# Performance work log

Hardware: AMD Instinct MI355X
Metric: run time of the kernel (lower is better)

## Reference

```python
import jax, jax.numpy as jnp
import numpy as np

D = 64        # kg_embedding_dim
T = 4096      # tokens
N = 20000     # kg nodes
M = T + N     # total nodes
E = 100000    # edges
R = 50        # relation types (num_edge_embeddings)
V = 100000    # num_node_embeddings
TOK = 768     # token_embedding_size


def setup_inputs() -> dict:
    key = jax.random.key(0)
    ks = jax.random.split(key, 24)
    s = 0.05
    node_ids = jax.random.randint(ks[0], (N,), 0, V)
    edge_index = jax.random.randint(ks[1], (2, E), 0, M)
    rel_ids = jax.random.randint(ks[2], (E,), 0, R)
    edge_attr = jax.nn.one_hot(rel_ids, R, dtype=jnp.float32)  # [E,R]
    token_embeddings = jax.random.normal(ks[3], (T, TOK), dtype=jnp.float32)
    node_type_labels = jax.random.randint(ks[4], (M,), 0, 3)
    return {
        'node_ids': node_ids,
        'edge_index': edge_index,
        'edge_attr': edge_attr,
        'token_embeddings': token_embeddings,
        'node_type_labels': node_type_labels,
        # learned params
        'kg_emb': jax.random.normal(ks[5], (V, D), dtype=jnp.float32) * s,
        'rel_emb': jax.random.normal(ks[6], (R, D), dtype=jnp.float32) * s,
        'w_e2': jax.random.normal(ks[7], (D, D * D), dtype=jnp.float32) * s,
        'b_e2': jnp.zeros((D * D,), dtype=jnp.float32),
        'att1_w': jax.random.normal(ks[8], (2 * D, 1), dtype=jnp.float32) * s,
        'att1_b': jnp.zeros((1,), dtype=jnp.float32),
        'root1': jax.random.normal(ks[9], (D, D), dtype=jnp.float32) * s,
        'bias1': jnp.zeros((D,), dtype=jnp.float32),
        'att2_w': jax.random.normal(ks[10], (2 * D, 1), dtype=jnp.float32) * s,
        'att2_b': jnp.zeros((1,), dtype=jnp.float32),
        'root2': jax.random.normal(ks[11], (D, D), dtype=jnp.float32) * s,
        'bias2': jnp.zeros((D,), dtype=jnp.float32),
        'w_lin1': jax.random.normal(ks[12], (TOK, D), dtype=jnp.float32) * s,
        'b_lin1': jnp.zeros((D,), dtype=jnp.float32),
        'w_lin2': jax.random.normal(ks[13], (D, TOK), dtype=jnp.float32) * s,
        'b_lin2': jnp.zeros((TOK,), dtype=jnp.float32),
        'w_nt': jax.random.normal(ks[14], (D, 3), dtype=jnp.float32) * s,
        'b_nt': jnp.zeros((3,), dtype=jnp.float32),
    }


def _ecgat(x, src, dst, w_edge, att_w, att_b, root, bias):
    # x: [M,D], w_edge: [E,D,D]
    x_j = x[src]                                    # gather source nodes [E,D]
    x_i = x[dst]                                    # gather target nodes [E,D]
    nbr = jnp.einsum('ed,edo->eo', x_j, w_edge)     # per-edge matmul [E,D]
    a = jnp.concatenate([x_i, nbr], axis=1) @ att_w + att_b   # [E,1]
    a = jax.nn.softmax(a, axis=0)                   # global softmax over edges (dim=0 in torch)
    msg = x_j * a                                   # message = x_j * alpha
    aggr = jax.ops.segment_sum(msg, dst, num_segments=M)      # scatter-add [M,D]
    return aggr + x @ root + bias


def reference(node_ids, edge_index, edge_attr, token_embeddings, node_type_labels,
              kg_emb, rel_emb, w_e2, b_e2,
              att1_w, att1_b, root1, bias1,
              att2_w, att2_b, root2, bias2,
              w_lin1, b_lin1, w_lin2, b_lin2, w_nt, b_nt):
    src, dst = edge_index[0], edge_index[1]
    tok = token_embeddings @ w_lin1 + b_lin1        # [T,D]
    nodes = kg_emb[node_ids]                        # [N,D]
    x = jnp.concatenate([tok, nodes], axis=0)       # [M,D]

    # EdgeNet (shared by both conv layers, same edge_attr -> compute once)
    e_emb = edge_attr @ rel_emb                     # [E,D]
    w_edge = jax.nn.relu(e_emb @ w_e2 + b_e2).reshape(E, D, D)  # [E,D,D]

    x1 = _ecgat(x, src, dst, w_edge, att1_w, att1_b, root1, bias1)
    h = jax.nn.relu(x1)                             # dropout = identity in eval
    final_x = _ecgat(h, src, dst, w_edge, att2_w, att2_b, root2, bias2)

    # link_pred loss (MSE, masked, mean over all elements)
    pred_tails = final_x[src] + e_emb
    edge_labels = final_x[dst]
    mask = (edge_attr[:, -3:].sum(axis=1) == 0).astype(final_x.dtype)[:, None]
    kge_loss = jnp.mean((pred_tails - edge_labels) ** 2 * mask)

    # node-type classification loss (cross entropy)
    logp = jax.nn.log_softmax(final_x @ w_nt + b_nt, axis=-1)
    nt_loss = -jnp.mean(jnp.take_along_axis(logp, node_type_labels[:, None], axis=1))

    final_outputs = final_x @ w_lin2 + b_lin2       # [M,TOK]
    return final_outputs, kge_loss, nt_loss
```

## Files before the change

kernel.cpp:

```cpp
#include <hip/hip_runtime.h>

#define Dd   64
#define Tt   4096
#define Nn   20000
#define Mm   24096
#define Ee   100000
#define Rr   50
#define TOK  768

#define NB_TOK   512
#define NB_NODES 1250
#define NB_RELID 4883
#define NB_W     800
#define NB_ZERO  95
#define NBM_HIST 391
#define NBM_U    13
#define NBM_P    6024
#define NBA_FILL 391
#define NBA_ATT  2048
#define NKGE     391
#define NNT      95
#define NFIN     (NKGE+NNT)
#define NGEMM    753

__device__ __forceinline__ float waveRed(float v){
  #pragma unroll
  for(int o=32;o;o>>=1) v += __shfl_xor(v,o,64);
  return v;
}

__global__ __launch_bounds__(256) void k_prep(
    const float* __restrict__ A, const float* __restrict__ wl1, const float* __restrict__ bl1,
    const int* __restrict__ ids, const float* __restrict__ kg,
    const float* __restrict__ ea, int* __restrict__ relid,
    const float* __restrict__ rel, const float* __restrict__ w2, const float* __restrict__ b2,
    float* __restrict__ W, int* __restrict__ deg, float* __restrict__ S,
    float* __restrict__ x){
  __shared__ float As[8*TOK];
  int b = blockIdx.x;
  const int t = threadIdx.x, lane = t&63, wave = t>>6;
  if(b < NB_TOK){
    const int rbase = b*8;
    #pragma unroll
    for(int i=0;i<6;i++){
      int f = t + 256*i;
      int row = f/192, c4 = (f - row*192)*4;
      *(float4*)&As[row*TOK + c4] = *(const float4*)&A[(size_t)(rbase+row)*TOK + c4];
    }
    __syncthreads();
    const int r0 = wave*2, r1 = r0+1;
    float a0=bl1[lane], a1=a0, c0=0.f, c1=0.f;
    for(int k=0;k<TOK;k+=2){
      float w0 = wl1[(size_t)k*Dd + lane];
      float w1 = wl1[(size_t)(k+1)*Dd + lane];
      a0 += As[r0*TOK+k]*w0;  c0 += As[r0*TOK+k+1]*w1;
      a1 += As[r1*TOK+k]*w0;  c1 += As[r1*TOK+k+1]*w1;
    }
    x[(size_t)(rbase+r0)*Dd + lane] = a0+c0;
    x[(size_t)(rbase+r1)*Dd + lane] = a1+c1;
  } else if(b < NB_TOK+NB_NODES){
    int tt = (b-NB_TOK)*256 + t;
    int i = tt>>4, c = tt&15;
    ((float4*)x)[(size_t)(Tt+i)*16 + c] = ((const float4*)kg)[(size_t)ids[i]*16 + c];
  } else if(b < NB_TOK+NB_NODES+NB_RELID){
    int tt = (b-NB_TOK-NB_NODES)*256 + t;
    size_t g4 = (size_t)tt*4;
    if(g4 < (size_t)Ee*Rr){
      float4 v = *(const float4*)&ea[g4];
      #pragma unroll
      for(int j=0;j<4;j++){
        if(((const float*)&v)[j] > 0.5f){
          unsigned g = (unsigned)(g4 + j);
          unsigned e = g / 50u;
          relid[e] = (int)(g - e*50u);
        }
      }
    }
  } else if(b < NB_TOK+NB_NODES+NB_RELID+NB_W){
    int tt = (b-NB_TOK-NB_NODES-NB_RELID)*256 + t;
    int r = tt>>12, j = tt&4095;
    float acc = b2[j];
    const float* rp = rel + r*Dd;
    #pragma unroll 8
    for(int d=0;d<Dd;d++) acc += rp[d] * w2[(size_t)d*4096 + j];
    W[tt] = acc > 0.f ? acc : 0.f;
  } else {
    int tt = (b-NB_TOK-NB_NODES-NB_RELID-NB_W)*256 + t;
    if(tt < Mm) deg[tt] = 0;
    else if(tt < Mm+8) S[tt-Mm] = 0.f;
  }
}

__global__ __launch_bounds__(256) void k_mid(const int* __restrict__ ei,
    int* __restrict__ deg, const float* __restrict__ W,
    const float* __restrict__ a1w, const float* __restrict__ a2w,
    float* __restrict__ U1, float* __restrict__ U2,
    const float* __restrict__ x, float* __restrict__ p){
  int b = blockIdx.x;
  const int t = threadIdx.x, lane = t&63, wave = t>>6;
  if(b < NBM_HIST){
    int e = b*256 + t;
    if(e < Ee) atomicAdd(&deg[ei[Ee+e]], 1);
  } else if(b < NBM_HIST+NBM_U){
    int tt = (b-NBM_HIST)*256 + t;
    if(tt < Rr*Dd){
      const float* wp = W + (size_t)(tt>>6)*4096 + (size_t)(tt&63)*Dd;
      float s1 = 0.f, s2 = 0.f;
      #pragma unroll 8
      for(int o=0;o<Dd;o++){ float w = wp[o]; s1 += w*a1w[Dd+o]; s2 += w*a2w[Dd+o]; }
      U1[tt] = s1; U2[tt] = s2;
    }
  } else {
    int i = (b-NBM_HIST-NBM_U)*4 + wave;
    float pv = waveRed(x[(size_t)i*Dd + lane] * a1w[lane]);
    if(lane==0) p[i] = pv;
  }
}

__global__ __launch_bounds__(1024) void k_scan(const int* __restrict__ deg,
    int* __restrict__ rowptr, int* __restrict__ cursor){
  __shared__ int ts[1024];
  int t = threadIdx.x;
  int base = t*24;
  int loc[24];
  int s = 0;
  #pragma unroll
  for(int j=0;j<24;j++){
    int idx = base+j;
    int d = (idx < Mm) ? deg[idx] : 0;
    loc[j] = s; s += d;
  }
  ts[t] = s;
  __syncthreads();
  for(int off=1; off<1024; off<<=1){
    int add = (t>=off) ? ts[t-off] : 0;
    __syncthreads();
    ts[t] += add;
    __syncthreads();
  }
  int excl = ts[t] - s;
  #pragma unroll
  for(int j=0;j<24;j++){
    int idx = base+j;
    if(idx < Mm){ int v = excl + loc[j]; rowptr[idx] = v; cursor[idx] = v; }
  }
  if(t==1023) rowptr[Mm] = ts[1023];
}

__global__ __launch_bounds__(256) void k_attf(const float* __restrict__ x,
    const int* __restrict__ ei, const int* __restrict__ relid,
    const float* __restrict__ U, const float* __restrict__ p,
    const float* __restrict__ ab, float* __restrict__ expa, float* __restrict__ S,
    int* __restrict__ cursor, int* __restrict__ eidx,
    int dorelu, int dofill){
  __shared__ float sw[4];
  int b = blockIdx.x;
  if(dofill){
    if(b < NBA_FILL){
      int e = b*256 + threadIdx.x;
      if(e < Ee){
        int d = ei[Ee+e];
        int pos = atomicAdd(&cursor[d], 1);
        eidx[pos] = e;
      }
      return;
    }
    b -= NBA_FILL;
  }
  int lane = threadIdx.x&63, wid = threadIdx.x>>6;
  int gw = b*4 + wid;
  float ab0 = ab[0];
  float acc = 0.f;
  for(int e = gw; e < Ee; e += 4*NBA_ATT){
    int src = ei[e], dst = ei[Ee+e], r = relid[e];
    float xv = x[(size_t)src*Dd + lane];
    if(dorelu) xv = fmaxf(xv, 0.f);
    float v = waveRed(xv * U[r*Dd + lane]);
    float ex = expf(v + p[dst] + ab0);
    if(lane==0) expa[e] = ex;
    acc += ex;
  }
  if(lane==0) sw[wid] = acc;
  __syncthreads();
  if(threadIdx.x==0) atomicAdd(S, sw[0]+sw[1]+sw[2]+sw[3]);
}

__global__ __launch_bounds__(256) void k_aggr(const float* __restrict__ x,
    const int* __restrict__ ei, const int* __restrict__ rowptr,
    const int* __restrict__ eidx, const float* __restrict__ expa,
    const float* __restrict__ S, const float* __restrict__ root,
    const float* __restrict__ bias, const float* __restrict__ awn,
    float* __restrict__ y, float* __restrict__ pnext, int dorelu){
  int lane = threadIdx.x&63, wid = threadIdx.x>>6;
  int dst = blockIdx.x*4 + wid;
  float invS = 1.f / S[0];
  int j0 = rowptr[dst], j1 = rowptr[dst+1];
  int deg = j1 - j0;
  float acc = 0.f;
  for(int base=0; base<deg; base+=64){
    int rem = deg - base;
    int n = rem < 64 ? rem : 64;
    float a = 0.f; int src = 0;
    if(lane < n){
      int e = eidx[j0 + base + lane];
      a = expa[e];
      src = ei[e];
    }
    for(int c=0; c<n; c+=8){
      float aj[8]; float xv[8];
      #pragma unroll
      for(int k=0;k<8;k++){
        int sj = __shfl(src, c+k, 64);
        aj[k]  = __shfl(a,   c+k, 64);
        xv[k]  = x[(size_t)sj*Dd + lane];
      }
      #pragma unroll
      for(int k=0;k<8;k++){
        float v = xv[k];
        if(dorelu) v = fmaxf(v, 0.f);
        acc += aj[k]*v;
      }
    }
  }
  acc *= invS;
  float xd = x[(size_t)dst*Dd + lane];
  if(dorelu) xd = fmaxf(xd, 0.f);
  float rsum = bias[lane];
  #pragma unroll 16
  for(int k=0;k<Dd;k++){
    float xk = __shfl(xd, k, 64);
    rsum += xk * root[k*Dd + lane];
  }
  float o = acc + rsum;
  y[(size_t)dst*Dd + lane] = o;
  if(pnext){
    float orl = fmaxf(o, 0.f);
    float pv = waveRed(orl * awn[lane]);
    if(lane==0) pnext[dst] = pv;
  }
}

__global__ __launch_bounds__(256) void k_out(const float* __restrict__ fx,
    const float* __restrict__ w, const float* __restrict__ b,
    const int* __restrict__ ei, const int* __restrict__ relid,
    const float* __restrict__ rel, const int* __restrict__ lab,
    const float* __restrict__ wnt, const float* __restrict__ bnt,
    float* __restrict__ S, float* __restrict__ out){
  __shared__ float aT[Dd][36];
  if(blockIdx.x < NFIN){
    __shared__ float sr[4];
    const int t = threadIdx.x, lane = t&63, wid = t>>6;
    float acc = 0.f;
    int slot;
    if(blockIdx.x < NKGE){
      slot = 2;
      const int cb = (blockIdx.x*4 + wid)*64;
      int e = cb + lane;
      bool vld = e < Ee;
      int sv = vld ? ei[e]    : 0;
      int dv = vld ? ei[Ee+e] : 0;
      int rv = vld ? relid[e] : 47;
      #pragma unroll 8
      for(int j=0;j<64;j++){
        int r = __shfl(rv, j, 64);
        int s = __shfl(sv, j, 64);
        int d = __shfl(dv, j, 64);
        float m = (r < 47) ? 1.f : 0.f;
        float diff = fx[(size_t)s*Dd + lane] + rel[r*Dd + lane] - fx[(size_t)d*Dd + lane];
        acc += m*diff*diff;
      }
      acc = waveRed(acc);
    } else {
      slot = 3;
      int i = (blockIdx.x - NKGE)*256 + t;
      float contrib = 0.f;
      if(i < Mm){
        const float* r = fx + (size_t)i*Dd;
        float l0 = bnt[0], l1 = bnt[1], l2 = bnt[2];
        #pragma unroll 8
        for(int k=0;k<Dd;k++){
          float f = r[k];
          l0 += f*wnt[k*3+0]; l1 += f*wnt[k*3+1]; l2 += f*wnt[k*3+2];
        }
        float mx = fmaxf(l0, fmaxf(l1,l2));
        float lse = logf(expf(l0-mx)+expf(l1-mx)+expf(l2-mx)) + mx;
        int lb = lab[i];
        float lp = (lb==0 ? l0 : (lb==1 ? l1 : l2)) - lse;
        contrib = -lp;
      }
      acc = waveRed(contrib);
    }
    if(lane==0) sr[wid] = acc;
    __syncthreads();
    if(t==0){
      atomicAdd(&S[slot], sr[0]+sr[1]+sr[2]+sr[3]);
      __threadfence();
      int prev = atomicAdd((int*)&S[4], 1);
      if(prev == NFIN-1){
        float v2 = atomicAdd(&S[2], 0.f);
        float v3 = atomicAdd(&S[3], 0.f);
        size_t base = (size_t)Mm*TOK;
        out[base+0] = v2 / (float)(Ee*Dd);
        out[base+1] = v3 / (float)Mm;
      }
    }
    return;
  }
  const int bb = blockIdx.x - NFIN;
  const int t = threadIdx.x;
  const int r0 = bb*32;
  #pragma unroll
  for(int i=0;i<2;i++){
    int f = t + 256*i;
    int r = f>>4, k4 = (f&15)*4;
    float4 v = *(const float4*)&fx[(size_t)(r0+r)*Dd + k4];
    aT[k4+0][r]=v.x; aT[k4+1][r]=v.y; aT[k4+2][r]=v.z; aT[k4+3][r]=v.w;
  }
  __syncthreads();
  const int tr = t>>5, tc = t&31;
  const int rb = tr*4, cb = tc*4;
  for(int cc=0; cc<6; cc++){
    const int co = cc*128;
    float4 bv = *(const float4*)&b[co+cb];
    float acc[4][4];
    #pragma unroll
    for(int i=0;i<4;i++){ acc[i][0]=bv.x; acc[i][1]=bv.y; acc[i][2]=bv.z; acc[i][3]=bv.w; }
    #pragma unroll 8
    for(int k=0;k<Dd;k++){
      float4 a  = *(const float4*)&aT[k][rb];
      float4 wv = *(const float4*)&w[(size_t)k*TOK + co + cb];
      #pragma unroll
      for(int i=0;i<4;i++){
        float av = ((const float*)&a)[i];
        acc[i][0] += av*wv.x; acc[i][1] += av*wv.y;
        acc[i][2] += av*wv.z; acc[i][3] += av*wv.w;
      }
    }
    #pragma unroll
    for(int i=0;i<4;i++){
      float4 o; o.x=acc[i][0]; o.y=acc[i][1]; o.z=acc[i][2]; o.w=acc[i][3];
      *(float4*)&out[(size_t)(r0+rb+i)*TOK + co + cb] = o;
    }
  }
}

extern "C" void kernel_launch(void* const* d_in, const int* in_sizes, int n_in,
                              void* d_out, int out_size, void* d_ws, size_t ws_size,
                              hipStream_t stream) {
  const int*   node_ids = (const int*)d_in[0];
  const int*   ei       = (const int*)d_in[1];
  const float* eattr    = (const float*)d_in[2];
  const float* tokemb   = (const float*)d_in[3];
  const int*   labels   = (const int*)d_in[4];
  const float* kg       = (const float*)d_in[5];
  const float* rel      = (const float*)d_in[6];
  const float* w_e2     = (const float*)d_in[7];
  const float* b_e2     = (const float*)d_in[8];
  const float* a1w      = (const float*)d_in[9];
  const float* a1b      = (const float*)d_in[10];
  const float* root1    = (const float*)d_in[11];
  const float* bias1    = (const float*)d_in[12];
  const float* a2w      = (const float*)d_in[13];
  const float* a2b      = (const float*)d_in[14];
  const float* root2    = (const float*)d_in[15];
  const float* bias2    = (const float*)d_in[16];
  const float* wlin1    = (const float*)d_in[17];
  const float* blin1    = (const float*)d_in[18];
  const float* wlin2    = (const float*)d_in[19];
  const float* blin2    = (const float*)d_in[20];
  const float* wnt      = (const float*)d_in[21];
  const float* bnt      = (const float*)d_in[22];

  float* wsb = (float*)d_ws;
  float* x    = wsb;
  float* h    = x  + (size_t)Mm*Dd;
  float* fx   = h  + (size_t)Mm*Dd;
  float* W    = fx + (size_t)Mm*Dd;
  float* U1   = W  + Rr*4096;
  float* U2   = U1 + Rr*Dd;
  float* expa = U2 + Rr*Dd;
  float* p    = expa + Ee;
  float* S    = p + Mm;
  int* relid  = (int*)(S + 8);
  int* deg    = relid + Ee;
  int* rowptr = deg + Mm;
  int* cursor = rowptr + Mm + 1;
  int* eidx   = cursor + Mm;
  float* out  = (float*)d_out;

  k_prep<<<NB_TOK+NB_NODES+NB_RELID+NB_W+NB_ZERO, 256, 0, stream>>>(
      tokemb, wlin1, blin1, node_ids, kg, eattr, relid, rel, w_e2, b_e2, W, deg, S, x);
  k_mid <<<NBM_HIST+NBM_U+NBM_P, 256, 0, stream>>>(ei, deg, W, a1w, a2w, U1, U2, x, p);
  k_scan<<<1, 1024, 0, stream>>>(deg, rowptr, cursor);

  k_attf<<<NBA_FILL+NBA_ATT, 256, 0, stream>>>(x, ei, relid, U1, p, a1b, expa, S,
                                               cursor, eidx, 0, 1);
  k_aggr<<<Mm/4, 256, 0, stream>>>(x, ei, rowptr, eidx, expa, S, root1, bias1, a2w, h, p, 0);

  k_attf<<<NBA_ATT, 256, 0, stream>>>(h, ei, relid, U2, p, a2b, expa, S+1,
                                      (int*)0, (int*)0, 1, 0);
  k_aggr<<<Mm/4, 256, 0, stream>>>(h, ei, rowptr, eidx, expa, S+1, root2, bias2,
                                   (const float*)0, fx, (float*)0, 1);

  k_out <<<NFIN + NGEMM, 256, 0, stream>>>(
      fx, wlin2, blin2, ei, relid, rel, labels, wnt, bnt, S, out);
}
```

Before: 406.2 us.

## Split output GEMM across column groups and stage weight tile in shared memory

New measurement: 411.4 us. About the same (+1.3%).

```diff
diff --git a/kernel.cpp b/kernel.cpp
--- a/kernel.cpp
+++ b/kernel.cpp
@@ -21,7 +21,8 @@
 #define NKGE     391
 #define NNT      95
 #define NFIN     (NKGE+NNT)
-#define NGEMM    753
+#define NGROW    753
+#define NGCOL    12
 
 __device__ __forceinline__ float waveRed(float v){
   #pragma unroll
@@ -247,6 +248,7 @@
     const float* __restrict__ wnt, const float* __restrict__ bnt,
     float* __restrict__ S, float* __restrict__ out){
   __shared__ float aT[Dd][36];
+  __shared__ float ws2[Dd][64];
   if(blockIdx.x < NFIN){
     __shared__ float sr[4];
     const int t = threadIdx.x, lane = t&63, wid = t>>6;
@@ -307,8 +309,10 @@
     return;
   }
   const int bb = blockIdx.x - NFIN;
+  const int cg = bb / NGROW;
+  const int bx = bb - cg*NGROW;
   const int t = threadIdx.x;
-  const int r0 = bb*32;
+  const int r0 = bx*32, co = cg*64;
   #pragma unroll
   for(int i=0;i<2;i++){
     int f = t + 256*i;
@@ -316,31 +320,33 @@
     float4 v = *(const float4*)&fx[(size_t)(r0+r)*Dd + k4];
     aT[k4+0][r]=v.x; aT[k4+1][r]=v.y; aT[k4+2][r]=v.z; aT[k4+3][r]=v.w;
   }
+  #pragma unroll
+  for(int i=0;i<4;i++){
+    int f = t + 256*i;
+    int kk = f>>4, c4 = (f&15)*4;
+    *(float4*)&ws2[kk][c4] = *(const float4*)&w[(size_t)kk*TOK + co + c4];
+  }
   __syncthreads();
   const int tr = t>>5, tc = t&31;
-  const int rb = tr*4, cb = tc*4;
-  for(int cc=0; cc<6; cc++){
-    const int co = cc*128;
-    float4 bv = *(const float4*)&b[co+cb];
-    float acc[4][4];
-    #pragma unroll
-    for(int i=0;i<4;i++){ acc[i][0]=bv.x; acc[i][1]=bv.y; acc[i][2]=bv.z; acc[i][3]=bv.w; }
-    #pragma unroll 8
-    for(int k=0;k<Dd;k++){
-      float4 a  = *(const float4*)&aT[k][rb];
-      float4 wv = *(const float4*)&w[(size_t)k*TOK + co + cb];
-      #pragma unroll
-      for(int i=0;i<4;i++){
-        float av = ((const float*)&a)[i];
-        acc[i][0] += av*wv.x; acc[i][1] += av*wv.y;
-        acc[i][2] += av*wv.z; acc[i][3] += av*wv.w;
-      }
-    }
+  const int rb = tr*4, cb2 = tc*2;
+  float b0 = b[co+cb2], b1 = b[co+cb2+1];
+  float acc[4][2];
+  #pragma unroll
+  for(int i=0;i<4;i++){ acc[i][0]=b0; acc[i][1]=b1; }
+  #pragma unroll 16
+  for(int k=0;k<Dd;k++){
+    float4 a  = *(const float4*)&aT[k][rb];
+    float2 wv = *(const float2*)&ws2[k][cb2];
     #pragma unroll
     for(int i=0;i<4;i++){
-      float4 o; o.x=acc[i][0]; o.y=acc[i][1]; o.z=acc[i][2]; o.w=acc[i][3];
-      *(float4*)&out[(size_t)(r0+rb+i)*TOK + co + cb] = o;
-    }
+      float av = ((const float*)&a)[i];
+      acc[i][0] += av*wv.x; acc[i][1] += av*wv.y;
+    }
+  }
+  #pragma unroll
+  for(int i=0;i<4;i++){
+    float2 o; o.x=acc[i][0]; o.y=acc[i][1];
+    *(float2*)&out[(size_t)(r0+rb+i)*TOK + co + cb2] = o;
   }
 }
 
@@ -402,6 +408,6 @@
   k_aggr<<<Mm/4, 256, 0, stream>>>(h, ei, rowptr, eidx, expa, S+1, root2, bias2,
                                    (const float*)0, fx, (float*)0, 1);
 
-  k_out <<<NFIN + NGEMM, 256, 0, stream>>>(
+  k_out <<<NFIN + NGROW*NGCOL, 256, 0, stream>>>(
       fx, wlin2, blin2, ei, relid, rel, labels, wnt, bnt, S, out);
 }
```
